# Kernel tuning notes

Hardware: AMD Instinct MI355X
Metric: run time of the kernel (lower is better)

## Reference

```python
import jax, jax.numpy as jnp
import numpy as np

DIM = 64
NUM_GRAPHS = 500
N_NODES = 50000
N_EDGES = 100000
PROC_STEPS = 6  # both conv/GRU iterations and Set2Set processing steps


def setup_inputs() -> dict:
    key = jax.random.key(0)
    ks = jax.random.split(key, 32)
    d = DIM
    f = lambda k, shape, s=0.05: jax.random.normal(k, shape, dtype=jnp.float32) * s
    return {
        "x": jax.random.normal(ks[0], (N_NODES, 3), dtype=jnp.float32),
        "edge_index": jax.random.randint(ks[1], (2, N_EDGES), 0, N_NODES),
        "edge_attr": jax.random.uniform(ks[2], (N_EDGES, 7), dtype=jnp.float32),
        "batch": jnp.sort(jax.random.randint(ks[3], (N_NODES,), 0, NUM_GRAPHS)),
        "lin0_w": f(ks[4], (d, 3)), "lin0_b": f(ks[5], (d,)),
        "mlp_w1": f(ks[6], (128, 7)), "mlp_b1": f(ks[7], (128,)),
        "mlp_w2": f(ks[8], (d * d, 128)), "mlp_b2": f(ks[9], (d * d,)),
        "conv_root": f(ks[10], (d, d)), "conv_bias": f(ks[11], (d,)),
        "gru_w_ih": f(ks[12], (3 * d, d)), "gru_w_hh": f(ks[13], (3 * d, d)),
        "gru_b_ih": f(ks[14], (3 * d,)), "gru_b_hh": f(ks[15], (3 * d,)),
        "s2s_w_ih": f(ks[16], (4 * d, 2 * d)), "s2s_w_hh": f(ks[17], (4 * d, d)),
        "s2s_b_ih": f(ks[18], (4 * d,)), "s2s_b_hh": f(ks[19], (4 * d,)),
        "mem_w_ih": f(ks[20], (8 * d, 2 * d)), "mem_w_hh": f(ks[21], (8 * d, 2 * d)),
        "mem_b_ih": f(ks[22], (8 * d,)), "mem_b_hh": f(ks[23], (8 * d,)),
        "lin1_w": f(ks[24], (d, 2 * d)), "lin1_b": f(ks[25], (d,)),
        "lin3_w": f(ks[26], (1, d)), "lin3_b": f(ks[27], (1,)),
    }


def _forward(x, edge_index, edge_attr, batch,
             lin0_w, lin0_b, mlp_w1, mlp_b1, mlp_w2, mlp_b2,
             conv_root, conv_bias,
             gru_w_ih, gru_w_hh, gru_b_ih, gru_b_hh,
             s2s_w_ih, s2s_w_hh, s2s_b_ih, s2s_b_hh,
             mem_w_ih, mem_w_hh, mem_b_ih, mem_b_hh,
             lin1_w, lin1_b, lin3_w, lin3_b):
    d = lin0_w.shape[0]
    n = x.shape[0]
    B = NUM_GRAPHS
    src, dst = edge_index[0], edge_index[1]

    # NNConv edge-conditioned weights (edge_attr is constant across iterations)
    h1 = jax.nn.relu(edge_attr @ mlp_w1.T + mlp_b1)          # [E,128]
    Wmat = (h1 @ mlp_w2.T + mlp_b2).reshape(-1, d, d)        # [E,d_in,d_out]
    deg = jnp.maximum(
        jax.ops.segment_sum(jnp.ones_like(dst, jnp.float32), dst, n), 1.0)

    out = jax.nn.relu(x @ lin0_w.T + lin0_b)                  # [N,d]
    h = out                                                   # GRU hidden, [N,d]
    for _ in range(PROC_STEPS):
        # NNConv: per-edge matmul, mean scatter, root weight + bias
        msg = jnp.einsum('ei,eio->eo', out[src], Wmat)        # [E,d]
        agg = jax.ops.segment_sum(msg, dst, n) / deg[:, None]
        m = jax.nn.relu(agg + out @ conv_root + conv_bias)
        # GRU step (seq len 1)
        gi = m @ gru_w_ih.T + gru_b_ih
        gh = h @ gru_w_hh.T + gru_b_hh
        i_r, i_z, i_n = jnp.split(gi, 3, axis=-1)
        h_r, h_z, h_n = jnp.split(gh, 3, axis=-1)
        r = jax.nn.sigmoid(i_r + h_r)
        z = jax.nn.sigmoid(i_z + h_z)
        nn_ = jnp.tanh(i_n + r * h_n)
        h = (1.0 - z) * nn_ + z * h
        out = h

    # Set2Set pooling (processing_steps = 6)
    hs = jnp.zeros((B, d), dtype=x.dtype)
    cs = jnp.zeros((B, d), dtype=x.dtype)
    q_star = jnp.zeros((B, 2 * d), dtype=x.dtype)
    for _ in range(PROC_STEPS):
        gates = q_star @ s2s_w_ih.T + s2s_b_ih + hs @ s2s_w_hh.T + s2s_b_hh
        ii, ff, gg, oo = jnp.split(gates, 4, axis=-1)
        cs = jax.nn.sigmoid(ff) * cs + jax.nn.sigmoid(ii) * jnp.tanh(gg)
        hs = jax.nn.sigmoid(oo) * jnp.tanh(cs)
        q = hs                                                # [B,d]
        e = jnp.sum(out * q[batch], axis=-1)                  # [N]
        e_max = jax.ops.segment_max(e, batch, B)
        a = jnp.exp(e - e_max[batch])
        a = a / jax.ops.segment_sum(a, batch, B)[batch]       # segment softmax
        r_ = jax.ops.segment_sum(a[:, None] * out, batch, B)  # [B,d]
        q_star = jnp.concatenate([q, r_], axis=-1)            # [B,2d]

    # memory LSTM: seq len 1, zero initial state => h0 @ w_hh == 0
    gates = q_star @ mem_w_ih.T + mem_b_ih + mem_b_hh         # [B,8d]
    ii, ff, gg, oo = jnp.split(gates, 4, axis=-1)
    c = jax.nn.sigmoid(ii) * jnp.tanh(gg)
    hmem = jax.nn.sigmoid(oo) * jnp.tanh(c)

    o1 = jax.nn.relu(hmem @ lin1_w.T + lin1_b)
    v = o1 @ lin3_w.T + lin3_b                                # [B,1]
    return v, hmem[None], c[None]


def reference(x, edge_index, edge_attr, batch,
              lin0_w, lin0_b, mlp_w1, mlp_b1, mlp_w2, mlp_b2,
              conv_root, conv_bias,
              gru_w_ih, gru_w_hh, gru_b_ih, gru_b_hh,
              s2s_w_ih, s2s_w_hh, s2s_b_ih, s2s_b_hh,
              mem_w_ih, mem_w_hh, mem_b_ih, mem_b_hh,
              lin1_w, lin1_b, lin3_w, lin3_b):
    return _forward(x, edge_index, edge_attr, batch,
                    lin0_w, lin0_b, mlp_w1, mlp_b1, mlp_w2, mlp_b2,
                    conv_root, conv_bias,
                    gru_w_ih, gru_w_hh, gru_b_ih, gru_b_hh,
                    s2s_w_ih, s2s_w_hh, s2s_b_ih, s2s_b_hh,
                    mem_w_ih, mem_w_hh, mem_b_ih, mem_b_hh,
                    lin1_w, lin1_b, lin3_w, lin3_b)
```

## Files before the change

### kernel.cpp

```cpp
#include <hip/hip_runtime.h>

#define NN 50000
#define NE 100000
#define NB 500
#define NEP 100096
#define NKF 136
#define CKF 4

typedef _Float16 half2_t __attribute__((ext_vector_type(2)));
typedef _Float16 half8_t __attribute__((ext_vector_type(8)));
typedef float f32x16 __attribute__((ext_vector_type(16)));

union F8U { half8_t v; uint4 u; };

__device__ __forceinline__ float sigm(float x){ return 1.0f/(1.0f + __expf(-x)); }
__device__ __forceinline__ unsigned short f16u(float f){
  _Float16 h = (_Float16)f; return *(unsigned short*)&h;
}


__global__ void k_gstart(const int* __restrict__ batch, int* __restrict__ gst){
  int g = blockIdx.x*blockDim.x + threadIdx.x;
  if (g > NB) return;
  if (g == NB){ gst[g] = NN; return; }
  int lo=0, hi=NN;
  while (lo < hi){ int mid=(lo+hi)>>1; if (batch[mid] < g) lo = mid+1; else hi = mid; }
  gst[g] = lo;
}

__global__ void k_deg(const int* __restrict__ dst, float* __restrict__ deg){
  int e = blockIdx.x*blockDim.x + threadIdx.x;
  if (e < NE) atomicAdd(&deg[dst[e]], 1.0f);
}

__global__ void k_rdeg(float* __restrict__ deg){
  int i = blockIdx.x*blockDim.x + threadIdx.x;
  if (i < NN) deg[i] = 1.0f / fmaxf(deg[i], 1.0f);
}

__global__ void k_h1T(const float* __restrict__ ea, const float* __restrict__ w1,
                      const float* __restrict__ b1, _Float16* __restrict__ h1T){
  int e = blockIdx.x*256 + threadIdx.x;
  int j = blockIdx.y;
  if (e >= NE) return;
  float s;
  if (j == 128){
    s = 1.0f;
  } else {
    const float* a = ea + (size_t)e*7;
    const float* wr = w1 + j*7;
    s = b1[j];
    #pragma unroll
    for (int k=0;k<7;k++) s = fmaf(a[k], wr[k], s);
    s = fmaxf(s, 0.0f);
  }
  h1T[(size_t)j*NEP + e] = (_Float16)s;
}

__global__ void k_lin0(const float* __restrict__ x, const float* __restrict__ w,
                       const float* __restrict__ b, float* __restrict__ hbuf){
  int idx = blockIdx.x*blockDim.x + threadIdx.x;
  if (idx >= NN*64) return;
  int n = idx >> 6, o = idx & 63;
  const float* xr = x + n*3;
  const float* wr = w + o*3;
  float s = b[o] + xr[0]*wr[0] + xr[1]*wr[1] + xr[2]*wr[2];
  hbuf[idx] = fmaxf(s, 0.0f);
}

__global__ void k_prepB(const float* __restrict__ w2, const float* __restrict__ b2,
                        _Float16* __restrict__ B2s){
  int idx = blockIdx.x*blockDim.x + threadIdx.x;
  if (idx >= NKF*4096) return;
  int kf = idx >> 12, r = idx & 4095, o = r >> 6, i = r & 63;
  float v = (kf < 128) ? w2[(size_t)(i*64+o)*128 + kf] : (kf == 128 ? b2[i*64+o] : 0.0f);
  int byt = (o*128 + i*2) ^ ((o&7)<<4);
  *(unsigned short*)((char*)B2s + (size_t)kf*8192 + byt) = f16u(v);
}

__global__ void k_prepW(const float* __restrict__ root, const float* __restrict__ wih,
                        const float* __restrict__ whh, _Float16* __restrict__ Wg){
  int idx = blockIdx.x*blockDim.x + threadIdx.x;
  if (idx >= 28672) return;
  if (idx < 4096){
    int o = idx >> 6, k = idx & 63;
    int byt = (o*128 + k*2) ^ ((o&7)<<4);
    *(unsigned short*)((char*)Wg + byt) = f16u(root[k*64 + o]);
  } else {
    int x = idx - 4096;
    int o = x >> 7, k = x & 127;
    float v = (k < 64) ? wih[o*64 + k] : whh[o*64 + (k-64)];
    int byt = (o*256 + k*2) ^ ((o&7)<<4);
    *(unsigned short*)((char*)Wg + 8192 + byt) = f16u(v);
  }
}

__global__ __launch_bounds__(256) void k_msgemm2(
    const _Float16* __restrict__ h1T, const _Float16* __restrict__ B2s,
    const float* __restrict__ hbuf, const int* __restrict__ src,
    const int* __restrict__ dst, float* __restrict__ agg){
  __shared__ __align__(16) _Float16 Bsh[CKF*4096];
  __shared__ __align__(16) _Float16 h1sh[CKF*256];
  __shared__ int dst_s[256];
  const int t = threadIdx.x;
  const int lane = t & 63, wv = t >> 6;
  const int hi = lane >> 5, lm = lane & 31;
  const int we = wv >> 1, wo = wv & 1;
  const int o0 = wo * 32;
  const int e0 = blockIdx.x * 256;
  {
    int eg = e0 + t;
    dst_s[t] = (eg < NE) ? dst[eg] : -1;
  }
  half8_t xa[4][4];
  #pragma unroll
  for (int tt=0; tt<4; ++tt){
    int eg = e0 + tt*64 + we*32 + lm;
    int sidx = (eg < NE) ? src[eg] : 0;
    const float4* xr = (const float4*)(hbuf + (size_t)sidx*64);
    #pragma unroll
    for (int q=0;q<4;++q){
      float4 a = xr[q*4 + hi*2];
      float4 b = xr[q*4 + hi*2 + 1];
      half8_t h;
      h[0]=(_Float16)a.x; h[1]=(_Float16)a.y; h[2]=(_Float16)a.z; h[3]=(_Float16)a.w;
      h[4]=(_Float16)b.x; h[5]=(_Float16)b.y; h[6]=(_Float16)b.z; h[7]=(_Float16)b.w;
      xa[tt][q] = h;
    }
  }
  f32x16 acc[4] = {};
  for (int c = 0; c < NKF/CKF; ++c){
    __syncthreads();
    const char* gB = (const char*)B2s + (size_t)c*(CKF*8192);
    #pragma unroll 4
    for (int r=0;r<8;++r){
      uint4 u = *(const uint4*)(gB + r*4096 + t*16);
      *(uint4*)((char*)Bsh + r*4096 + t*16) = u;
    }
    if (t < 128){
      int rr = t >> 5, cc = t & 31;
      uint4 u = *(const uint4*)((const char*)h1T + ((size_t)(c*CKF+rr)*NEP + (size_t)e0)*2 + cc*16);
      *(uint4*)((char*)h1sh + rr*512 + cc*16) = u;
    }
    __syncthreads();
    #pragma unroll
    for (int kf=0; kf<CKF; ++kf){
      _Float16 hv0 = h1sh[kf*256 +       we*32 + lm];
      _Float16 hv1 = h1sh[kf*256 +  64 + we*32 + lm];
      _Float16 hv2 = h1sh[kf*256 + 128 + we*32 + lm];
      _Float16 hv3 = h1sh[kf*256 + 192 + we*32 + lm];
      half8_t b0 = {hv0,hv0,hv0,hv0,hv0,hv0,hv0,hv0};
      half8_t b1 = {hv1,hv1,hv1,hv1,hv1,hv1,hv1,hv1};
      half8_t b2_ = {hv2,hv2,hv2,hv2,hv2,hv2,hv2,hv2};
      half8_t b3 = {hv3,hv3,hv3,hv3,hv3,hv3,hv3,hv3};
      #pragma unroll
      for (int q=0;q<4;++q){
        F8U bf;
        int byt = (((o0+lm)*128 + q*32 + hi*16) ^ ((lm&7)<<4));
        bf.u = *(const uint4*)((const char*)Bsh + kf*8192 + byt);
        acc[0] = __builtin_amdgcn_mfma_f32_32x32x16_f16(xa[0][q]*b0, bf.v, acc[0], 0,0,0);
        acc[1] = __builtin_amdgcn_mfma_f32_32x32x16_f16(xa[1][q]*b1, bf.v, acc[1], 0,0,0);
        acc[2] = __builtin_amdgcn_mfma_f32_32x32x16_f16(xa[2][q]*b2_, bf.v, acc[2], 0,0,0);
        acc[3] = __builtin_amdgcn_mfma_f32_32x32x16_f16(xa[3][q]*b3, bf.v, acc[3], 0,0,0);
      }
    }
  }
  #pragma unroll
  for (int tt=0;tt<4;++tt){
    #pragma unroll
    for (int r=0;r<16;++r){
      int row = (r&3) + 8*(r>>2) + 4*hi;
      int d = dst_s[tt*64 + we*32 + row];
      if (d >= 0) atomicAdd(&agg[(size_t)d*64 + o0 + lm], acc[tt][r]);
    }
  }
}

__global__ __launch_bounds__(256) void k_node2(
    const float* __restrict__ agg, const float* __restrict__ rdeg,
    float* __restrict__ hbuf, const _Float16* __restrict__ Wg,
    const float* __restrict__ cbias, const float* __restrict__ bih,
    const float* __restrict__ bhh){
  __shared__ __align__(16) _Float16 WB[28672];
  __shared__ __align__(16) _Float16 mT[4][2048];
  const int t = threadIdx.x;
  const int lane = t & 63, wv = t >> 6;
  const int hi = lane >> 5, lm = lane & 31;
  #pragma unroll 2
  for (int r=0;r<14;++r){
    uint4 u = *(const uint4*)((const char*)Wg + r*4096 + t*16);
    *(uint4*)((char*)WB + r*4096 + t*16) = u;
  }
  const int n0 = blockIdx.x*128 + wv*32;
  half8_t ah[4];
  {
    int nr = min(n0 + lm, NN-1);
    const float4* hr = (const float4*)(hbuf + (size_t)nr*64);
    #pragma unroll
    for (int q=0;q<4;++q){
      float4 a = hr[q*4 + hi*2];
      float4 b = hr[q*4 + hi*2 + 1];
      half8_t h;
      h[0]=(_Float16)a.x; h[1]=(_Float16)a.y; h[2]=(_Float16)a.z; h[3]=(_Float16)a.w;
      h[4]=(_Float16)b.x; h[5]=(_Float16)b.y; h[6]=(_Float16)b.z; h[7]=(_Float16)b.w;
      ah[q] = h;
    }
  }
  __syncthreads();
  f32x16 am[2] = {};
  #pragma unroll
  for (int q=0;q<4;++q){
    #pragma unroll
    for (int ot=0;ot<2;++ot){
      int o = ot*32 + lm;
      F8U bf;
      bf.u = *(const uint4*)((const char*)WB + ((o*128 + q*32 + hi*16) ^ ((o&7)<<4)));
      am[ot] = __builtin_amdgcn_mfma_f32_32x32x16_f16(ah[q], bf.v, am[ot], 0,0,0);
    }
  }
  #pragma unroll
  for (int ot=0;ot<2;++ot){
    int col = ot*32 + lm;
    float cb = cbias[col];
    #pragma unroll
    for (int r=0;r<16;++r){
      int row = (r&3) + 8*(r>>2) + 4*hi;
      int n = min(n0 + row, NN-1);
      float mv = fmaxf(fmaf(agg[(size_t)n*64 + col], rdeg[n], am[ot][r] + cb), 0.0f);
      *(unsigned short*)((char*)&mT[wv][0] + ((row*128 + col*2) ^ ((row&7)<<4))) = f16u(mv);
    }
  }
  __syncthreads();
  half8_t amf[4];
  #pragma unroll
  for (int q=0;q<4;++q){
    F8U v;
    v.u = *(const uint4*)((const char*)&mT[wv][0] + ((lm*128 + q*32 + hi*16) ^ ((lm&7)<<4)));
    amf[q] = v.v;
  }
  f32x16 aF[4] = {}; f32x16 aIN[2] = {}; f32x16 aHN[2] = {};
  const char* WGp = (const char*)WB + 8192;
  #pragma unroll
  for (int q=0;q<4;++q){
    #pragma unroll
    for (int ot=0;ot<4;++ot){
      int o = ot*32 + lm;
      F8U bf; bf.u = *(const uint4*)(WGp + ((o*256 + q*32 + hi*16) ^ ((o&7)<<4)));
      aF[ot] = __builtin_amdgcn_mfma_f32_32x32x16_f16(amf[q], bf.v, aF[ot], 0,0,0);
    }
    #pragma unroll
    for (int j=0;j<2;++j){
      int o = (4+j)*32 + lm;
      F8U bf; bf.u = *(const uint4*)(WGp + ((o*256 + q*32 + hi*16) ^ ((o&7)<<4)));
      aIN[j] = __builtin_amdgcn_mfma_f32_32x32x16_f16(amf[q], bf.v, aIN[j], 0,0,0);
    }
  }
  #pragma unroll
  for (int q=0;q<4;++q){
    #pragma unroll
    for (int ot=0;ot<4;++ot){
      int o = ot*32 + lm;
      F8U bf; bf.u = *(const uint4*)(WGp + ((o*256 + 128 + q*32 + hi*16) ^ ((o&7)<<4)));
      aF[ot] = __builtin_amdgcn_mfma_f32_32x32x16_f16(ah[q], bf.v, aF[ot], 0,0,0);
    }
    #pragma unroll
    for (int j=0;j<2;++j){
      int o = (4+j)*32 + lm;
      F8U bf; bf.u = *(const uint4*)(WGp + ((o*256 + 128 + q*32 + hi*16) ^ ((o&7)<<4)));
      aHN[j] = __builtin_amdgcn_mfma_f32_32x32x16_f16(ah[q], bf.v, aHN[j], 0,0,0);
    }
  }
  #pragma unroll
  for (int j=0;j<2;++j){
    int col = j*32 + lm;
    float br = bih[col] + bhh[col];
    float bz = bih[64+col] + bhh[64+col];
    float bin = bih[128+col], bhn = bhh[128+col];
    #pragma unroll
    for (int r=0;r<16;++r){
      int row = (r&3) + 8*(r>>2) + 4*hi;
      int n = n0 + row;
      int nc = min(n, NN-1);
      float rg = sigm(aF[j][r] + br);
      float z  = sigm(aF[2+j][r] + bz);
      float nn_ = tanhf(aIN[j][r] + bin + rg*(aHN[j][r] + bhn));
      float hold = hbuf[(size_t)nc*64 + col];
      float hnew = (1.0f - z)*nn_ + z*hold;
      if (n < NN) hbuf[(size_t)n*64 + col] = hnew;
    }
  }
}

__global__ __launch_bounds__(256) void k_tail(
    const float* __restrict__ hbuf, const int* __restrict__ gst,
    float* __restrict__ ebuf,
    const float* __restrict__ swih, const float* __restrict__ swhh,
    const float* __restrict__ sbih, const float* __restrict__ sbhh,
    const float* __restrict__ mwih, const float* __restrict__ mbih,
    const float* __restrict__ mbhh, const float* __restrict__ l1w,
    const float* __restrict__ l1b, const float* __restrict__ l3w,
    const float* __restrict__ l3b, float* __restrict__ out){
  const int g = blockIdx.x, t = threadIdx.x;
  const int start = gst[g], end = gst[g+1];
  const int lane = t & 63, wv = t >> 6;
  __shared__ float qsh[128];
  __shared__ float hsh[64], csh[64];
  __shared__ float gat[512];
  __shared__ float red[256];
  __shared__ float rpart[4][64];
  __shared__ float hm[128], o1[64];
  if (t < 128) qsh[t] = 0.f;
  if (t < 64){ hsh[t] = 0.f; csh[t] = 0.f; }
  for (int it = 0; it < 6; ++it){
    __syncthreads();
    {
      float s = sbih[t] + sbhh[t];
      const float* wr = swih + (size_t)t*128;
      #pragma unroll 4
      for (int k=0;k<128;k++) s = fmaf(qsh[k], wr[k], s);
      const float* hr = swhh + (size_t)t*64;
      #pragma unroll 4
      for (int k=0;k<64;k++) s = fmaf(hsh[k], hr[k], s);
      gat[t] = s;
    }
    __syncthreads();
    if (t < 64){
      float ii = gat[t], ff = gat[64+t], gg = gat[128+t], oo = gat[192+t];
      float c = sigm(ff)*csh[t] + sigm(ii)*tanhf(gg);
      csh[t] = c;
      hsh[t] = sigm(oo)*tanhf(c);
    }
    __syncthreads();
    float lmax = -1e30f;
    for (int n = start + t; n < end; n += 256){
      const float4* row = (const float4*)(hbuf + (size_t)n*64);
      float s = 0.f;
      #pragma unroll
      for (int k=0;k<16;k++){
        float4 v = row[k];
        s += v.x*hsh[4*k] + v.y*hsh[4*k+1] + v.z*hsh[4*k+2] + v.w*hsh[4*k+3];
      }
      ebuf[n] = s;
      lmax = fmaxf(lmax, s);
    }
    red[t] = lmax; __syncthreads();
    for (int o2=128; o2>0; o2>>=1){ if (t<o2) red[t] = fmaxf(red[t], red[t+o2]); __syncthreads(); }
    const float gmax = red[0]; __syncthreads();
    float lsum = 0.f;
    for (int n = start + t; n < end; n += 256){
      float a = __expf(ebuf[n] - gmax);
      ebuf[n] = a;
      lsum += a;
    }
    red[t] = lsum; __syncthreads();
    for (int o2=128; o2>0; o2>>=1){ if (t<o2) red[t] += red[t+o2]; __syncthreads(); }
    const float inv = (red[0] > 0.f) ? 1.0f/red[0] : 0.f;
    float racc = 0.f;
    for (int n = start + wv; n < end; n += 4)
      racc = fmaf(ebuf[n], hbuf[(size_t)n*64 + lane], racc);
    rpart[wv][lane] = racc;
    __syncthreads();
    if (t < 64){
      qsh[t] = hsh[t];
      qsh[64+t] = (rpart[0][t] + rpart[1][t] + rpart[2][t] + rpart[3][t]) * inv;
    }
  }
  __syncthreads();
  for (int r = t; r < 512; r += 256){
    float s = mbih[r] + mbhh[r];
    const float* wr = mwih + (size_t)r*128;
    #pragma unroll 4
    for (int k=0;k<128;k++) s = fmaf(qsh[k], wr[k], s);
    gat[r] = s;
  }
  __syncthreads();
  if (t < 128){
    float c = sigm(gat[t]) * tanhf(gat[256+t]);
    float hmem = sigm(gat[384+t]) * tanhf(c);
    hm[t] = hmem;
    out[500 + g*128 + t] = hmem;
    out[64500 + g*128 + t] = c;
  }
  __syncthreads();
  if (t < 64){
    float s = l1b[t];
    const float* wr = l1w + (size_t)t*128;
    #pragma unroll 4
    for (int k=0;k<128;k++) s = fmaf(hm[k], wr[k], s);
    o1[t] = fmaxf(s, 0.f);
  }
  __syncthreads();
  if (t == 0){
    float v = l3b[0];
    for (int k=0;k<64;k++) v = fmaf(o1[k], l3w[k], v);
    out[g] = v;
  }
}

extern "C" void kernel_launch(void* const* d_in, const int* in_sizes, int n_in,
                              void* d_out, int out_size, void* d_ws, size_t ws_size,
                              hipStream_t stream){
  (void)in_sizes; (void)n_in;
  const float* x     = (const float*)d_in[0];
  const int*   eidx  = (const int*)d_in[1];
  const float* eattr = (const float*)d_in[2];
  const int*   batch = (const int*)d_in[3];
  const float* lin0w = (const float*)d_in[4];
  const float* lin0b = (const float*)d_in[5];
  const float* mw1   = (const float*)d_in[6];
  const float* mb1   = (const float*)d_in[7];
  const float* mw2   = (const float*)d_in[8];
  const float* mb2   = (const float*)d_in[9];
  const float* convr = (const float*)d_in[10];
  const float* convb = (const float*)d_in[11];
  const float* gwih  = (const float*)d_in[12];
  const float* gwhh  = (const float*)d_in[13];
  const float* gbih  = (const float*)d_in[14];
  const float* gbhh  = (const float*)d_in[15];
  const float* swih  = (const float*)d_in[16];
  const float* swhh  = (const float*)d_in[17];
  const float* sbih  = (const float*)d_in[18];
  const float* sbhh  = (const float*)d_in[19];
  const float* mwih  = (const float*)d_in[20];
  const float* mbih  = (const float*)d_in[22];
  const float* mbhh  = (const float*)d_in[23];
  const float* l1w   = (const float*)d_in[24];
  const float* l1b   = (const float*)d_in[25];
  const float* l3w   = (const float*)d_in[26];
  const float* l3b   = (const float*)d_in[27];
  float* out = (float*)d_out;
  const int* src = eidx;
  const int* dstp = eidx + NE;

  size_t off = 0;
  auto take = [&](size_t bytes)->void*{
    void* p = (void*)((char*)d_ws + off);
    off = (off + bytes + 255) & ~(size_t)255;
    return p;
  };
  _Float16* h1T = (_Float16*)take((size_t)NKF*NEP*2);
  _Float16* B2s = (_Float16*)take((size_t)NKF*8192);
  _Float16* Wg  = (_Float16*)take((size_t)28672*2);
  float* hbuf = (float*)take((size_t)NN*64*4);
  float* agg  = (float*)take((size_t)NN*64*4);
  float* deg  = (float*)take((size_t)NN*4);
  float* ebuf = (float*)take((size_t)NN*4);
  int*   gst  = (int*)take((size_t)(NB+1)*4);

  if (off > ws_size){
    hipMemsetAsync(d_out, 0, (size_t)out_size*4, stream);
    return;
  }

  hipMemsetAsync(h1T, 0, (size_t)NKF*NEP*2, stream);
  hipMemsetAsync(deg, 0, (size_t)NN*4, stream);
  k_gstart<<<4, 128, 0, stream>>>(batch, gst);
  k_deg<<<(NE+255)/256, 256, 0, stream>>>(dstp, deg);
  k_rdeg<<<(NN+255)/256, 256, 0, stream>>>(deg);
  k_h1T<<<dim3((NE+255)/256, 129), 256, 0, stream>>>(eattr, mw1, mb1, h1T);
  k_lin0<<<NN*64/256, 256, 0, stream>>>(x, lin0w, lin0b, hbuf);
  k_prepB<<<(NKF*4096+255)/256, 256, 0, stream>>>(mw2, mb2, B2s);
  k_prepW<<<(28672+255)/256, 256, 0, stream>>>(convr, gwih, gwhh, Wg);

  for (int step = 0; step < 6; ++step){
    hipMemsetAsync(agg, 0, (size_t)NN*64*4, stream);
    k_msgemm2<<<NEP/256, 256, 0, stream>>>(h1T, B2s, hbuf, src, dstp, agg);
    k_node2<<<(NN+127)/128, 256, 0, stream>>>(agg, deg, hbuf, Wg, convb, gbih, gbhh);
  }

  k_tail<<<NB, 256, 0, stream>>>(hbuf, gst, ebuf, swih, swhh, sbih, sbhh,
                                 mwih, mbih, mbhh, l1w, l1b, l3w, l3b, out);
}
```

Before: 1.235 ms.

## Fold Set2Set LSTM weights and stage them in LDS for tail kernel

Set2Set's q_star starts with h, so the input and recurrent weight matrices are pre-summed into one 256x128 matrix by a new prep kernel. The tail kernel copies that folded matrix into padded shared memory once per graph block and reuses it across the six steps instead of re-reading global memory. Block reductions move from a shared-memory tree to wave shuffles, and the final matvecs use float4 loads. The cost is a 132KB shared allocation per block, which caps occupancy, plus a 128KB copy into shared memory per block.

```diff
diff --git a/kernel.cpp b/kernel.cpp
--- a/kernel.cpp
+++ b/kernel.cpp
@@ -93,6 +93,16 @@
     int byt = (o*256 + k*2) ^ ((o&7)<<4);
     *(unsigned short*)((char*)Wg + 8192 + byt) = f16u(v);
   }
+}
+
+__global__ void k_prepS(const float* __restrict__ swih, const float* __restrict__ swhh,
+                        float* __restrict__ cw){
+  int idx = blockIdx.x*blockDim.x + threadIdx.x;
+  if (idx >= 256*128) return;
+  int t = idx >> 7, k = idx & 127;
+  float v = swih[(size_t)t*128 + k];
+  if (k < 64) v += swhh[(size_t)t*64 + k];
+  cw[idx] = v;
 }
 
 __global__ __launch_bounds__(256) void k_msgemm2(
@@ -293,85 +303,110 @@
 
 __global__ __launch_bounds__(256) void k_tail(
     const float* __restrict__ hbuf, const int* __restrict__ gst,
-    float* __restrict__ ebuf,
-    const float* __restrict__ swih, const float* __restrict__ swhh,
+    float* __restrict__ ebuf, const float* __restrict__ cw,
     const float* __restrict__ sbih, const float* __restrict__ sbhh,
     const float* __restrict__ mwih, const float* __restrict__ mbih,
     const float* __restrict__ mbhh, const float* __restrict__ l1w,
     const float* __restrict__ l1b, const float* __restrict__ l3w,
     const float* __restrict__ l3b, float* __restrict__ out){
+  __shared__ float Ws[256*129];
+  __shared__ __align__(16) float hsr[128];
+  __shared__ float hs[64], cs[64];
+  __shared__ float gat[512];
+  __shared__ float red[4];
+  __shared__ __align__(16) float rpart[4][64];
+  __shared__ __align__(16) float hm[128];
+  __shared__ __align__(16) float o1[64];
   const int g = blockIdx.x, t = threadIdx.x;
   const int start = gst[g], end = gst[g+1];
   const int lane = t & 63, wv = t >> 6;
-  __shared__ float qsh[128];
-  __shared__ float hsh[64], csh[64];
-  __shared__ float gat[512];
-  __shared__ float red[256];
-  __shared__ float rpart[4][64];
-  __shared__ float hm[128], o1[64];
-  if (t < 128) qsh[t] = 0.f;
-  if (t < 64){ hsh[t] = 0.f; csh[t] = 0.f; }
+  for (int idx = t; idx < 256*128; idx += 256){
+    int r = idx >> 7, k = idx & 127;
+    Ws[r*129 + k] = cw[idx];
+  }
+  if (t < 128) hsr[t] = 0.f;
+  if (t < 64){ hs[t] = 0.f; cs[t] = 0.f; }
+  const float bs = sbih[t] + sbhh[t];
+  __syncthreads();
   for (int it = 0; it < 6; ++it){
-    __syncthreads();
     {
-      float s = sbih[t] + sbhh[t];
-      const float* wr = swih + (size_t)t*128;
-      #pragma unroll 4
-      for (int k=0;k<128;k++) s = fmaf(qsh[k], wr[k], s);
-      const float* hr = swhh + (size_t)t*64;
-      #pragma unroll 4
-      for (int k=0;k<64;k++) s = fmaf(hsh[k], hr[k], s);
+      float s = bs;
+      const float* wr = &Ws[t*129];
+      const float4* h4 = (const float4*)hsr;
+      #pragma unroll
+      for (int k4=0;k4<32;k4++){
+        float4 q = h4[k4];
+        s = fmaf(q.x, wr[4*k4],   s);
+        s = fmaf(q.y, wr[4*k4+1], s);
+        s = fmaf(q.z, wr[4*k4+2], s);
+        s = fmaf(q.w, wr[4*k4+3], s);
+      }
       gat[t] = s;
     }
     __syncthreads();
     if (t < 64){
       float ii = gat[t], ff = gat[64+t], gg = gat[128+t], oo = gat[192+t];
-      float c = sigm(ff)*csh[t] + sigm(ii)*tanhf(gg);
-      csh[t] = c;
-      hsh[t] = sigm(oo)*tanhf(c);
+      float c = sigm(ff)*cs[t] + sigm(ii)*tanhf(gg);
+      cs[t] = c;
+      hs[t] = sigm(oo)*tanhf(c);
     }
     __syncthreads();
     float lmax = -1e30f;
     for (int n = start + t; n < end; n += 256){
       const float4* row = (const float4*)(hbuf + (size_t)n*64);
-      float s = 0.f;
+      float sc = 0.f;
       #pragma unroll
       for (int k=0;k<16;k++){
         float4 v = row[k];
-        s += v.x*hsh[4*k] + v.y*hsh[4*k+1] + v.z*hsh[4*k+2] + v.w*hsh[4*k+3];
+        sc += v.x*hs[4*k] + v.y*hs[4*k+1] + v.z*hs[4*k+2] + v.w*hs[4*k+3];
       }
-      ebuf[n] = s;
-      lmax = fmaxf(lmax, s);
-    }
-    red[t] = lmax; __syncthreads();
-    for (int o2=128; o2>0; o2>>=1){ if (t<o2) red[t] = fmaxf(red[t], red[t+o2]); __syncthreads(); }
-    const float gmax = red[0]; __syncthreads();
+      ebuf[n] = sc;
+      lmax = fmaxf(lmax, sc);
+    }
+    #pragma unroll
+    for (int m=1;m<64;m<<=1) lmax = fmaxf(lmax, __shfl_xor(lmax, m));
+    if (lane == 0) red[wv] = lmax;
+    __syncthreads();
+    const float gmax = fmaxf(fmaxf(red[0],red[1]), fmaxf(red[2],red[3]));
+    __syncthreads();
     float lsum = 0.f;
     for (int n = start + t; n < end; n += 256){
       float a = __expf(ebuf[n] - gmax);
       ebuf[n] = a;
       lsum += a;
     }
-    red[t] = lsum; __syncthreads();
-    for (int o2=128; o2>0; o2>>=1){ if (t<o2) red[t] += red[t+o2]; __syncthreads(); }
-    const float inv = (red[0] > 0.f) ? 1.0f/red[0] : 0.f;
+    #pragma unroll
+    for (int m=1;m<64;m<<=1) lsum += __shfl_xor(lsum, m);
+    if (lane == 0) red[wv] = lsum;
+    __syncthreads();
+    const float tot = red[0]+red[1]+red[2]+red[3];
+    const float inv = (tot > 0.f) ? 1.0f/tot : 0.f;
     float racc = 0.f;
     for (int n = start + wv; n < end; n += 4)
       racc = fmaf(ebuf[n], hbuf[(size_t)n*64 + lane], racc);
     rpart[wv][lane] = racc;
     __syncthreads();
     if (t < 64){
-      qsh[t] = hsh[t];
-      qsh[64+t] = (rpart[0][t] + rpart[1][t] + rpart[2][t] + rpart[3][t]) * inv;
-    }
-  }
-  __syncthreads();
-  for (int r = t; r < 512; r += 256){
-    float s = mbih[r] + mbhh[r];
-    const float* wr = mwih + (size_t)r*128;
-    #pragma unroll 4
-    for (int k=0;k<128;k++) s = fmaf(qsh[k], wr[k], s);
-    gat[r] = s;
+      hsr[t] = hs[t];
+      hsr[64+t] = (rpart[0][t]+rpart[1][t]+rpart[2][t]+rpart[3][t]) * inv;
+    }
+    __syncthreads();
+  }
+  {
+    const float4* q4 = (const float4*)hsr;
+    #pragma unroll
+    for (int rr=0; rr<2; ++rr){
+      int r = t + rr*256;
+      const float4* wr = (const float4*)(mwih + (size_t)r*128);
+      float4 a = make_float4(0.f,0.f,0.f,0.f);
+      #pragma unroll
+      for (int k=0;k<32;k++){
+        float4 w = wr[k]; float4 q = q4[k];
+        a.x = fmaf(w.x,q.x,a.x); a.y = fmaf(w.y,q.y,a.y);
+        a.z = fmaf(w.z,q.z,a.z); a.w = fmaf(w.w,q.w,a.w);
+      }
+      gat[r] = a.x+a.y+a.z+a.w + mbih[r] + mbhh[r];
+    }
   }
   __syncthreads();
   if (t < 128){
@@ -383,11 +418,16 @@
   }
   __syncthreads();
   if (t < 64){
-    float s = l1b[t];
-    const float* wr = l1w + (size_t)t*128;
-    #pragma unroll 4
-    for (int k=0;k<128;k++) s = fmaf(hm[k], wr[k], s);
-    o1[t] = fmaxf(s, 0.f);
+    const float4* wr = (const float4*)(l1w + (size_t)t*128);
+    const float4* h4 = (const float4*)hm;
+    float4 a = make_float4(0.f,0.f,0.f,0.f);
+    #pragma unroll
+    for (int k=0;k<32;k++){
+      float4 w = wr[k]; float4 q = h4[k];
+      a.x = fmaf(w.x,q.x,a.x); a.y = fmaf(w.y,q.y,a.y);
+      a.z = fmaf(w.z,q.z,a.z); a.w = fmaf(w.w,q.w,a.w);
+    }
+    o1[t] = fmaxf(a.x+a.y+a.z+a.w + l1b[t], 0.f);
   }
   __syncthreads();
   if (t == 0){
@@ -441,6 +481,7 @@
   _Float16* h1T = (_Float16*)take((size_t)NKF*NEP*2);
   _Float16* B2s = (_Float16*)take((size_t)NKF*8192);
   _Float16* Wg  = (_Float16*)take((size_t)28672*2);
+  float* cw   = (float*)take((size_t)256*128*4);
   float* hbuf = (float*)take((size_t)NN*64*4);
   float* agg  = (float*)take((size_t)NN*64*4);
   float* deg  = (float*)take((size_t)NN*4);
@@ -461,6 +502,7 @@
   k_lin0<<<NN*64/256, 256, 0, stream>>>(x, lin0w, lin0b, hbuf);
   k_prepB<<<(NKF*4096+255)/256, 256, 0, stream>>>(mw2, mb2, B2s);
   k_prepW<<<(28672+255)/256, 256, 0, stream>>>(convr, gwih, gwhh, Wg);
+  k_prepS<<<128, 256, 0, stream>>>(swih, swhh, cw);
 
   for (int step = 0; step < 6; ++step){
     hipMemsetAsync(agg, 0, (size_t)NN*64*4, stream);
@@ -468,6 +510,6 @@
     k_node2<<<(NN+127)/128, 256, 0, stream>>>(agg, deg, hbuf, Wg, convb, gbih, gbhh);
   }
 
-  k_tail<<<NB, 256, 0, stream>>>(hbuf, gst, ebuf, swih, swhh, sbih, sbhh,
+  k_tail<<<NB, 256, 0, stream>>>(hbuf, gst, ebuf, cw, sbih, sbhh,
                                  mwih, mbih, mbhh, l1w, l1b, l3w, l3b, out);
 }
```

New measurement: 1.171 ms. 5.2% less time.
